# Optimization experiments

Measured on AMD Instinct MI355X. Metric: run time of the kernel, lower is better.

## Reference

```python
import jax, jax.numpy as jnp
import numpy as np

S_NUM, E_NUM, K, B = 50000, 20000, 128, 8192
N = S_NUM + E_NUM
N_EDGES = 1000000
LAYERS = 3


def setup_inputs() -> dict:
    key = jax.random.key(0)
    ks = jax.random.split(key, 16)
    return {
        "stu_emb": jax.random.normal(ks[0], (S_NUM, K), jnp.float32),
        "exer_emb": jax.random.normal(ks[1], (E_NUM, K), jnp.float32),
        "kn_emb": jax.random.normal(ks[2], (K, K), jnp.float32),
        "disc_emb": jax.random.normal(ks[3], (E_NUM, 1), jnp.float32),
        "right_W": jax.random.normal(ks[4], (LAYERS, K, K), jnp.float32) * (1.0 / np.sqrt(K)),
        "wrong_W": jax.random.normal(ks[5], (LAYERS, K, K), jnp.float32) * (1.0 / np.sqrt(K)),
        "right_ci": jax.random.uniform(ks[6], (N, 1), jnp.float32),
        "right_cj": jax.random.uniform(ks[7], (N, 1), jnp.float32),
        "wrong_ci": jax.random.uniform(ks[8], (N, 1), jnp.float32),
        "wrong_cj": jax.random.uniform(ks[9], (N, 1), jnp.float32),
        "right_edges": jax.random.randint(ks[10], (2, N_EDGES), 0, N, jnp.int64),
        "wrong_edges": jax.random.randint(ks[11], (2, N_EDGES), 0, N, jnp.int64),
        "student_id": jax.random.randint(ks[12], (B,), 0, S_NUM, jnp.int64),
        "exercise_id": jax.random.randint(ks[13], (B,), 0, E_NUM, jnp.int64),
    }


def _gcmc_layer(feat, W, cj, ci, src, dst, n_nodes):
    # dense projection + src-side normalizer (dropout is identity in eval)
    h = (feat @ W) * cj                    # [N, K]
    # copy_u/sum message passing: scatter-add messages to destination nodes
    agg = jax.ops.segment_sum(h[src], dst, num_segments=n_nodes)  # [N, K]
    return agg * ci


def _graph_forward(feat, Ws, ci, cj, edges, n_nodes):
    src, dst = edges[0], edges[1]
    for i in range(Ws.shape[0]):
        feat = _gcmc_layer(feat, Ws[i], cj, ci, src, dst, n_nodes)
    return feat


def reference(stu_emb, exer_emb, kn_emb, disc_emb, right_W, wrong_W,
              right_ci, right_cj, wrong_ci, wrong_cj,
              right_edges, wrong_edges, student_id, exercise_id):
    n_students = stu_emb.shape[0]
    n_nodes = stu_emb.shape[0] + exer_emb.shape[0]
    all_weight = jnp.concatenate([stu_emb, exer_emb], axis=0)  # [N, K]
    w1 = _graph_forward(all_weight, right_W, right_ci, right_cj, right_edges, n_nodes)
    w2 = _graph_forward(all_weight, wrong_W, wrong_ci, wrong_cj, wrong_edges, n_nodes)
    stu_forward = w1[:n_students] + w2[:n_students]
    exer_forward = w1[n_students:] + w2[n_students:]
    batch_stu_ts = stu_forward[student_id]      # [B, K]
    batch_exer_ts = exer_forward[exercise_id]   # [B, K]
    disc_ts = disc_emb[exercise_id]             # [B, 1]
    knowledge_ts = kn_emb                       # [K, K]
    return (batch_stu_ts, batch_exer_ts, disc_ts, knowledge_ts)
```

## Files before the change

kernel.cpp:

```cpp
#include <hip/hip_runtime.h>
#include <hip/hip_bf16.h>
#include <stdint.h>

#define S_NUM 50000
#define E_NUM 20000
#define NNODE 70000
#define KDIM 128
#define BATCH 8192
#define NEDGE 1000000

#define NRANGE 128
#define RSZ 547
#define BUCKET_CAP 8448
#define RCAP 16672
#define CHUNK 8192
#define BINCAP 120
#define GR 256

typedef __attribute__((ext_vector_type(8))) short short8;
typedef __attribute__((ext_vector_type(4))) float f32x4;
typedef __attribute__((ext_vector_type(2))) float f32x2;

__device__ __forceinline__ float bf2f(ushort u) {
    union { uint32_t i; float f; } v; v.i = ((uint32_t)u) << 16; return v.f;
}
__device__ __forceinline__ ushort f2bf(float f) {
    union { uint32_t i; float f; } v; v.f = f;
    uint32_t r = v.i + 0x7fffu + ((v.i >> 16) & 1u);
    return (ushort)(r >> 16);
}
__device__ __forceinline__ f32x2 up2(uint32_t u) {
    union { uint32_t i; float f; } lo, hi;
    lo.i = u << 16; hi.i = u & 0xffff0000u;
    f32x2 r; r.x = lo.f; r.y = hi.f; return r;
}

__global__ void prepW_k(const float* __restrict__ rW, const float* __restrict__ wW,
                        ushort* __restrict__ ws, int* __restrict__ gbcnt) {
    if (blockIdx.x == 0 && threadIdx.x < 256) gbcnt[threadIdx.x] = 0;
    int i = blockIdx.x * blockDim.x + threadIdx.x;
    if (i >= 6 * 16384) return;
    int m = i >> 14, idx = i & 16383;
    const float* W = (m < 3) ? rW + m * 16384 : wW + (m - 3) * 16384;
    float x = W[idx];
    int k = idx >> 7, c = idx & 127;
    ushort hb = f2bf(x);
    ushort lb = f2bf(x - bf2f(hb));
    int off = ((c * 256 + 2 * k) ^ ((c & 7) << 4)) >> 1;
    ws[(size_t)m * 32768 + off] = hb;
    ws[(size_t)m * 32768 + 16384 + off] = lb;
}

__global__ __launch_bounds__(256) void bucket_k(const int* __restrict__ redge,
                                                const int* __restrict__ wedge,
                                                int* __restrict__ gbcnt,
                                                uint32_t* __restrict__ bpk) {
    __shared__ uint32_t lpk[NRANGE][BINCAP];
    __shared__ int lcnt[NRANGE];
    __shared__ int gbase[NRANGE];
    const int NB = (NEDGE + CHUNK - 1) / CHUNK;
    int bid = blockIdx.x;
    int graph = bid >= NB;
    int cb = graph ? bid - NB : bid;
    const int* eg = graph ? wedge : redge;
    int e0 = cb * CHUNK;
    int nthis = min(CHUNK, NEDGE - e0);
    for (int i = threadIdx.x; i < NRANGE; i += 256) lcnt[i] = 0;
    __syncthreads();
    for (int i = threadIdx.x; i < nthis; i += 256) {
        int s = eg[e0 + i];
        int d = eg[NEDGE + e0 + i];
        int b = d / RSZ;
        uint32_t p = ((uint32_t)(d - b * RSZ) << 17) | (uint32_t)s;
        int slot = atomicAdd(&lcnt[b], 1);
        if (slot < BINCAP) lpk[b][slot] = p;
        else {
            int gs = atomicAdd(&gbcnt[graph * NRANGE + b], 1);
            if (gs < BUCKET_CAP)
                bpk[(size_t)(graph * NRANGE + b) * BUCKET_CAP + gs] = p;
        }
    }
    __syncthreads();
    for (int b = threadIdx.x; b < NRANGE; b += 256) {
        int c = min(lcnt[b], BINCAP);
        lcnt[b] = c;
        gbase[b] = atomicAdd(&gbcnt[graph * NRANGE + b], c);
    }
    __syncthreads();
    for (int b = 0; b < NRANGE; ++b) {
        int c = lcnt[b];
        size_t base = (size_t)(graph * NRANGE + b) * BUCKET_CAP + gbase[b];
        for (int i = threadIdx.x; i < c; i += 256)
            if (gbase[b] + i < BUCKET_CAP) bpk[base + i] = lpk[b][i];
    }
}

__global__ __launch_bounds__(256) void build_k(const uint32_t* __restrict__ bpk,
                                               const int* __restrict__ gbcnt,
                                               int* __restrict__ rpb,
                                               int* __restrict__ rpe,
                                               int* __restrict__ csr) {
    __shared__ int lcnt[RSZ];
    __shared__ int lexcl[RSZ];
    __shared__ int pexcl[RSZ];
    __shared__ int lcur[RSZ];
    __shared__ int sliceB[BUCKET_CAP];
    __shared__ int wsum[4];
    __shared__ int s_carry;
    int combo = blockIdx.x;
    int graph = combo >> 7, grp = combo & (NRANGE - 1);
    int lo = grp * RSZ;
    int rsize = min(RSZ, NNODE - lo);
    int n = min(gbcnt[combo], BUCKET_CAP);
    const uint32_t* bp = bpk + (size_t)combo * BUCKET_CAP;
    int* rpbg = rpb + graph * NNODE;
    int* rpeg = rpe + graph * NNODE;
    int* og = csr + (size_t)combo * RCAP;
    const int rbase = combo * RCAP;
    int tid = threadIdx.x, lane = tid & 63, wid = tid >> 6;

    for (int i = tid; i < rsize; i += 256) lcnt[i] = 0;
    if (tid == 0) s_carry = 0;
    __syncthreads();
    for (int i = tid; i < n; i += 256)
        atomicAdd(&lcnt[bp[i] >> 17], 1);
    __syncthreads();
    for (int base = 0; base < rsize; base += 256) {
        int i = base + tid;
        int v = (i < rsize) ? lcnt[i] : 0;
        int incl = v;
        #pragma unroll
        for (int off = 1; off < 64; off <<= 1) {
            int t = __shfl_up(incl, off, 64);
            if (lane >= off) incl += t;
        }
        if (lane == 63) wsum[wid] = incl;
        __syncthreads();
        int carry = s_carry;
        if (wid == 0 && lane < 4) {
            int wv = wsum[lane];
            #pragma unroll
            for (int off = 1; off < 4; off <<= 1) {
                int t = __shfl_up(wv, off, 64);
                if (lane >= off) wv += t;
            }
            wsum[lane] = wv;
        }
        __syncthreads();
        int waveoff = (wid == 0) ? 0 : wsum[wid - 1];
        int excl = carry + waveoff + incl - v;
        if (i < rsize) { lexcl[i] = excl; lcur[i] = excl; }
        __syncthreads();
        if (tid == 0) s_carry = carry + wsum[3];
        __syncthreads();
    }
    if (tid == 0) s_carry = 0;
    __syncthreads();
    for (int base = 0; base < rsize; base += 256) {
        int i = base + tid;
        int v = (i < rsize) ? ((lcnt[i] + 15) & ~15) : 0;
        int incl = v;
        #pragma unroll
        for (int off = 1; off < 64; off <<= 1) {
            int t = __shfl_up(incl, off, 64);
            if (lane >= off) incl += t;
        }
        if (lane == 63) wsum[wid] = incl;
        __syncthreads();
        int carry = s_carry;
        if (wid == 0 && lane < 4) {
            int wv = wsum[lane];
            #pragma unroll
            for (int off = 1; off < 4; off <<= 1) {
                int t = __shfl_up(wv, off, 64);
                if (lane >= off) wv += t;
            }
            wsum[lane] = wv;
        }
        __syncthreads();
        int waveoff = (wid == 0) ? 0 : wsum[wid - 1];
        int excl = carry + waveoff + incl - v;
        if (i < rsize) pexcl[i] = excl;
        __syncthreads();
        if (tid == 0) s_carry = carry + wsum[3];
        __syncthreads();
    }
    for (int i = tid; i < rsize; i += 256) {
        int pc = (lcnt[i] + 15) & ~15;
        rpbg[lo + i] = rbase + pexcl[i];
        rpeg[lo + i] = rbase + pexcl[i] + pc;
    }
    for (int i = tid; i < n; i += 256) {
        uint32_t p = bp[i];
        int slot = atomicAdd(&lcur[p >> 17], 1);
        sliceB[slot] = (int)p;
    }
    __syncthreads();
    for (int i = tid; i < n; i += 256) {
        uint32_t p = (uint32_t)sliceB[i];
        int r = p >> 17;
        og[pexcl[r] + (i - lexcl[r])] = (int)(p & 0x1FFFFu);
    }
    for (int r = tid; r < rsize; r += 256) {
        int c = lcnt[r], pc = (c + 15) & ~15, b = pexcl[r];
        for (int j = c; j < pc; ++j) og[b + j] = NNODE;
    }
}

__global__ __launch_bounds__(256) void cvt1_k(const float* __restrict__ stu,
                                              const float* __restrict__ exer,
                                              const float* __restrict__ rcj,
                                              const float* __restrict__ wcj,
                                              uint4* __restrict__ featb,
                                              uint4* __restrict__ fcR,
                                              uint4* __restrict__ fcW,
                                              float* __restrict__ cjpR,
                                              float* __restrict__ cjpW) {
    const int main = NNODE * 16;
    const int total = main + 48 + 2 * (NNODE + 1);
    const uint4 z4 = {0, 0, 0, 0};
    for (int i = blockIdx.x * blockDim.x + threadIdx.x; i < total;
         i += gridDim.x * blockDim.x) {
        if (i < main) {
            int node = i >> 4;
            int qq = i & 15;
            const float4* src = (const float4*)((node < S_NUM)
                                  ? stu + (size_t)node * KDIM
                                  : exer + (size_t)(node - S_NUM) * KDIM);
            float4 a = src[qq * 2];
            float4 b = src[qq * 2 + 1];
            uint4 o;
            o.x = (uint32_t)f2bf(a.x) | ((uint32_t)f2bf(a.y) << 16);
            o.y = (uint32_t)f2bf(a.z) | ((uint32_t)f2bf(a.w) << 16);
            o.z = (uint32_t)f2bf(b.x) | ((uint32_t)f2bf(b.y) << 16);
            o.w = (uint32_t)f2bf(b.z) | ((uint32_t)f2bf(b.w) << 16);
            featb[i] = o;
        } else if (i < main + 48) {
            int j = i - main;
            if (j < 16)      featb[(size_t)NNODE * 16 + j] = z4;
            else if (j < 32) fcR[(size_t)NNODE * 16 + (j - 16)] = z4;
            else             fcW[(size_t)NNODE * 16 + (j - 32)] = z4;
        } else {
            int k = i - main - 48;
            if (k <= NNODE)  cjpR[k] = (k < NNODE) ? rcj[k] : 0.f;
            else {
                int m = k - (NNODE + 1);
                cjpW[m] = (m < NNODE) ? wcj[m] : 0.f;
            }
        }
    }
}

__global__ __launch_bounds__(256) void agg2_k(const uint4* __restrict__ fcR,
                                              const uint4* __restrict__ fcW,
                                              const float* __restrict__ cjR,
                                              const float* __restrict__ cjW,
                                              const int* __restrict__ rpb,
                                              const int* __restrict__ rpe,
                                              const int* __restrict__ csr,
                                              uint4* __restrict__ outR,
                                              uint4* __restrict__ outW,
                                              int useCj) {
    int gn = (blockIdx.x * blockDim.x + threadIdx.x) >> 6;
    if (gn >= 2 * NNODE) return;
    int graph = gn >= NNODE;
    int n = graph ? gn - NNODE : gn;
    const uint4* fc = graph ? fcW : fcR;
    const float* cjg = graph ? cjW : cjR;
    const int* rpbg = rpb + graph * NNODE;
    const int* rpeg = rpe + graph * NNODE;
    uint4* outp = graph ? outW : outR;

    int lane = threadIdx.x & 63;
    int rowgrp = lane >> 4, c16 = lane & 15;
    int beg = rpbg[n], end = rpeg[n];
    f32x2 acc0 = {0.f, 0.f}, acc1 = {0.f, 0.f}, acc2v = {0.f, 0.f}, acc3 = {0.f, 0.f};

    if (useCj) {
        for (int e = beg; e < end; e += 16) {
            int s0 = csr[e + rowgrp];
            int s1 = csr[e + 4 + rowgrp];
            int s2 = csr[e + 8 + rowgrp];
            int s3 = csr[e + 12 + rowgrp];
            uint4 u0 = fc[(size_t)s0 * 16 + c16];
            uint4 u1 = fc[(size_t)s1 * 16 + c16];
            uint4 u2 = fc[(size_t)s2 * 16 + c16];
            uint4 u3 = fc[(size_t)s3 * 16 + c16];
            float c0 = cjg[s0], c1 = cjg[s1], c2 = cjg[s2], c3 = cjg[s3];
            f32x2 v0 = {c0, c0}, v1 = {c1, c1}, v2 = {c2, c2}, v3 = {c3, c3};
            acc0 += v0 * up2(u0.x) + v1 * up2(u1.x) + v2 * up2(u2.x) + v3 * up2(u3.x);
            acc1 += v0 * up2(u0.y) + v1 * up2(u1.y) + v2 * up2(u2.y) + v3 * up2(u3.y);
            acc2v += v0 * up2(u0.z) + v1 * up2(u1.z) + v2 * up2(u2.z) + v3 * up2(u3.z);
            acc3 += v0 * up2(u0.w) + v1 * up2(u1.w) + v2 * up2(u2.w) + v3 * up2(u3.w);
        }
    } else {
        for (int e = beg; e < end; e += 16) {
            int s0 = csr[e + rowgrp];
            int s1 = csr[e + 4 + rowgrp];
            int s2 = csr[e + 8 + rowgrp];
            int s3 = csr[e + 12 + rowgrp];
            uint4 u0 = fc[(size_t)s0 * 16 + c16];
            uint4 u1 = fc[(size_t)s1 * 16 + c16];
            uint4 u2 = fc[(size_t)s2 * 16 + c16];
            uint4 u3 = fc[(size_t)s3 * 16 + c16];
            acc0 += (up2(u0.x) + up2(u1.x)) + (up2(u2.x) + up2(u3.x));
            acc1 += (up2(u0.y) + up2(u1.y)) + (up2(u2.y) + up2(u3.y));
            acc2v += (up2(u0.z) + up2(u1.z)) + (up2(u2.z) + up2(u3.z));
            acc3 += (up2(u0.w) + up2(u1.w)) + (up2(u2.w) + up2(u3.w));
        }
    }
    float a[8] = {acc0.x, acc0.y, acc1.x, acc1.y, acc2v.x, acc2v.y, acc3.x, acc3.y};
    #pragma unroll
    for (int j = 0; j < 8; ++j) {
        a[j] += __shfl_xor(a[j], 16, 64);
        a[j] += __shfl_xor(a[j], 32, 64);
    }
    if (rowgrp == 0) {
        uint4 o;
        o.x = (uint32_t)f2bf(a[0]) | ((uint32_t)f2bf(a[1]) << 16);
        o.y = (uint32_t)f2bf(a[2]) | ((uint32_t)f2bf(a[3]) << 16);
        o.z = (uint32_t)f2bf(a[4]) | ((uint32_t)f2bf(a[5]) << 16);
        o.w = (uint32_t)f2bf(a[6]) | ((uint32_t)f2bf(a[7]) << 16);
        outp[(size_t)n * 16 + c16] = o;
    }
}

__global__ __launch_bounds__(256) void gemm2_k(const ushort* __restrict__ AR,
                                               const ushort* __restrict__ AW,
                                               const ushort* __restrict__ wsR,
                                               const ushort* __restrict__ wsW,
                                               const float* __restrict__ rci,
                                               const float* __restrict__ rcj,
                                               const float* __restrict__ wci,
                                               const float* __restrict__ wcj,
                                               ushort* __restrict__ outR,
                                               ushort* __restrict__ outW,
                                               int mode) {
    const int halfBlocks = (NNODE + GR - 1) / GR;
    int graph = blockIdx.x >= halfBlocks;
    int bb = graph ? blockIdx.x - halfBlocks : blockIdx.x;
    const ushort* A = graph ? AW : AR;
    const ushort* wsm = graph ? wsW : wsR;
    const float* ci = graph ? wci : rci;
    const float* cj = graph ? wcj : rcj;
    ushort* outB = graph ? outW : outR;

    __shared__ ushort wt[32768];
    {
        const uint4* g = (const uint4*)wsm;
        uint4* l = (uint4*)wt;
        for (int i = threadIdx.x; i < 4096; i += 256) l[i] = g[i];
    }
    __syncthreads();

    int wid = threadIdx.x >> 6, lane = threadIdx.x & 63;
    int q = lane >> 4, l16 = lane & 15;
    int rbase = bb * GR + wid * 64;

    short8 z8 = {0, 0, 0, 0, 0, 0, 0, 0};
    short8 afr[4][4];
    #pragma unroll
    for (int t = 0; t < 4; ++t) {
        int row = rbase + t * 16 + l16;
        bool rok = row < NNODE;
        const short8* ar = (const short8*)(A + (size_t)row * KDIM);
        #pragma unroll
        for (int kb = 0; kb < 4; ++kb)
            afr[t][kb] = rok ? ar[kb * 4 + q] : z8;
    }
    float scal[4][4];
    #pragma unroll
    for (int t = 0; t < 4; ++t)
        #pragma unroll
        for (int b = 0; b < 4; ++b) {
            int r = rbase + t * 16 + q * 4 + b;
            scal[t][b] = (r < NNODE) ? (mode ? ci[r] * cj[r] : ci[r]) : 0.f;
        }

    #pragma unroll
    for (int cb = 0; cb < 8; ++cb) {
        int c = cb * 16 + l16;
        short8 bHi[4], bLo[4];
        #pragma unroll
        for (int kb = 0; kb < 4; ++kb) {
            int byte = (c * 256 + 2 * (kb * 32 + q * 8)) ^ ((c & 7) << 4);
            bHi[kb] = *(const short8*)((const char*)wt + byte);
            bLo[kb] = *(const short8*)((const char*)wt + 32768 + byte);
        }
        #pragma unroll
        for (int t = 0; t < 4; ++t) {
            f32x4 acc = {0.f, 0.f, 0.f, 0.f};
            #pragma unroll
            for (int kb = 0; kb < 4; ++kb) {
                acc = __builtin_amdgcn_mfma_f32_16x16x32_bf16(afr[t][kb], bHi[kb], acc, 0, 0, 0);
                acc = __builtin_amdgcn_mfma_f32_16x16x32_bf16(afr[t][kb], bLo[kb], acc, 0, 0, 0);
            }
            #pragma unroll
            for (int b = 0; b < 4; ++b) {
                int r = rbase + t * 16 + q * 4 + b;
                if (r < NNODE)
                    outB[(size_t)r * KDIM + c] = f2bf(acc[b] * scal[t][b]);
            }
        }
    }
}

__global__ void out_k(const ushort* __restrict__ w1, const ushort* __restrict__ w2,
                      const float* __restrict__ disc, const float* __restrict__ kn,
                      const int* __restrict__ sid, const int* __restrict__ eid,
                      float* __restrict__ out) {
    const int total = 2 * BATCH * KDIM + BATCH + KDIM * KDIM;
    for (int i = blockIdx.x * blockDim.x + threadIdx.x; i < total;
         i += gridDim.x * blockDim.x) {
        if (i < BATCH * KDIM) {
            int b = i >> 7, c = i & 127;
            size_t n = (size_t)sid[b];
            out[i] = bf2f(w1[n * KDIM + c]) + bf2f(w2[n * KDIM + c]);
        } else if (i < 2 * BATCH * KDIM) {
            int j = i - BATCH * KDIM;
            int b = j >> 7, c = j & 127;
            size_t n = (size_t)(S_NUM + eid[b]);
            out[i] = bf2f(w1[n * KDIM + c]) + bf2f(w2[n * KDIM + c]);
        } else if (i < 2 * BATCH * KDIM + BATCH) {
            out[i] = disc[eid[i - 2 * BATCH * KDIM]];
        } else {
            out[i] = kn[i - (2 * BATCH * KDIM + BATCH)];
        }
    }
}

static inline size_t align_up(size_t x) { return (x + 255) & ~(size_t)255; }

extern "C" void kernel_launch(void* const* d_in, const int* in_sizes, int n_in,
                              void* d_out, int out_size, void* d_ws, size_t ws_size,
                              hipStream_t stream) {
    const float* stu  = (const float*)d_in[0];
    const float* exer = (const float*)d_in[1];
    const float* kn   = (const float*)d_in[2];
    const float* disc = (const float*)d_in[3];
    const float* rW   = (const float*)d_in[4];
    const float* wW   = (const float*)d_in[5];
    const float* rci  = (const float*)d_in[6];
    const float* rcj  = (const float*)d_in[7];
    const float* wci  = (const float*)d_in[8];
    const float* wcj  = (const float*)d_in[9];
    const int* redge   = (const int*)d_in[10];
    const int* wedge   = (const int*)d_in[11];
    const int* sid     = (const int*)d_in[12];
    const int* eid     = (const int*)d_in[13];
    float* out         = (float*)d_out;

    char* p = (char*)d_ws;
    const size_t fB16 = align_up((size_t)(NNODE + 1) * KDIM * 2);
    ushort* featb = (ushort*)p; p += fB16;
    ushort* fcR = (ushort*)p; p += fB16;
    ushort* fcW = (ushort*)p; p += fB16;
    ushort* pR  = (ushort*)p; p += fB16;
    ushort* pW  = (ushort*)p; p += fB16;
    ushort* ws  = (ushort*)p; p += align_up((size_t)6 * 32768 * 2);
    int* gbcnt = (int*)p; p += align_up((size_t)256 * 4);
    int* rpb = (int*)p; p += align_up((size_t)2 * NNODE * 4);
    int* rpe = (int*)p; p += align_up((size_t)2 * NNODE * 4);
    int* csr = (int*)p; p += align_up((size_t)256 * RCAP * 4);
    float* cjpR = (float*)p; p += align_up((size_t)(NNODE + 1) * 4);
    float* cjpW = (float*)p; p += align_up((size_t)(NNODE + 1) * 4);
    uint32_t* bpk = (uint32_t*)pR;

    const int gemmBlocks2 = 2 * ((NNODE + GR - 1) / GR);
    const int aggBlocks2 = (2 * NNODE * 64) / 256;
    const int NB = (NEDGE + CHUNK - 1) / CHUNK;

    prepW_k<<<(6 * 16384 + 255) / 256, 256, 0, stream>>>(rW, wW, ws, gbcnt);
    bucket_k<<<2 * NB, 256, 0, stream>>>(redge, wedge, gbcnt, bpk);
    build_k<<<256, 256, 0, stream>>>(bpk, gbcnt, rpb, rpe, csr);
    cvt1_k<<<2048, 256, 0, stream>>>(stu, exer, rcj, wcj, (uint4*)featb,
                                     (uint4*)fcR, (uint4*)fcW, cjpR, cjpW);

    agg2_k<<<aggBlocks2, 256, 0, stream>>>((const uint4*)featb, (const uint4*)featb,
                                           cjpR, cjpW, rpb, rpe, csr,
                                           (uint4*)pR, (uint4*)pW, 1);
    gemm2_k<<<gemmBlocks2, 256, 0, stream>>>(pR, pW, ws + 0 * 32768, ws + 3 * 32768,
                                             rci, rcj, wci, wcj, fcR, fcW, 1);
    agg2_k<<<aggBlocks2, 256, 0, stream>>>((const uint4*)fcR, (const uint4*)fcW,
                                           nullptr, nullptr, rpb, rpe, csr,
                                           (uint4*)pR, (uint4*)pW, 0);
    gemm2_k<<<gemmBlocks2, 256, 0, stream>>>(pR, pW, ws + 1 * 32768, ws + 4 * 32768,
                                             rci, rcj, wci, wcj, fcR, fcW, 1);
    agg2_k<<<aggBlocks2, 256, 0, stream>>>((const uint4*)fcR, (const uint4*)fcW,
                                           nullptr, nullptr, rpb, rpe, csr,
                                           (uint4*)pR, (uint4*)pW, 0);
    gemm2_k<<<gemmBlocks2, 256, 0, stream>>>(pR, pW, ws + 2 * 32768, ws + 5 * 32768,
                                             rci, rcj, wci, wcj, fcR, fcW, 0);

    out_k<<<2048, 256, 0, stream>>>(fcR, fcW, disc, kn, sid, eid, out);
}
```

Measured before the change: 393.7 us.

## Fuse neighbor aggregation with per-node MFMA projection into one kernel per layer

Each layer previously ran a gather/aggregate kernel writing bf16 rows to global memory, then a separate GEMM kernel reading them back. The new aggemm_k has each wave aggregate 16 nodes (two at a time, interleaving their edge gathers for more memory parallelism), stage the results in a swizzled LDS tile, and immediately multiply by the layer weight with MFMA. Weights are now read from global memory instead of being copied into LDS per block. This removes one intermediate write and read plus three launches, but each wave does a small 16-row GEMM with weight reloads, and uneven node degrees within a wave may cause imbalance. Ping-pong buffers swap between pR/pW and fcR/fcW, so their padding rows are now zeroed as well.

Result: slower. 406.0 us (+3.1%).

```diff
diff --git a/kernel.cpp b/kernel.cpp
--- a/kernel.cpp
+++ b/kernel.cpp
@@ -15,7 +15,6 @@
 #define RCAP 16672
 #define CHUNK 8192
 #define BINCAP 120
-#define GR 256
 
 typedef __attribute__((ext_vector_type(8))) short short8;
 typedef __attribute__((ext_vector_type(4))) float f32x4;
@@ -214,10 +213,12 @@
                                               uint4* __restrict__ featb,
                                               uint4* __restrict__ fcR,
                                               uint4* __restrict__ fcW,
+                                              uint4* __restrict__ pR,
+                                              uint4* __restrict__ pW,
                                               float* __restrict__ cjpR,
                                               float* __restrict__ cjpW) {
     const int main = NNODE * 16;
-    const int total = main + 48 + 2 * (NNODE + 1);
+    const int total = main + 80 + 2 * (NNODE + 1);
     const uint4 z4 = {0, 0, 0, 0};
     for (int i = blockIdx.x * blockDim.x + threadIdx.x; i < total;
          i += gridDim.x * blockDim.x) {
@@ -235,13 +236,18 @@
             o.z = (uint32_t)f2bf(b.x) | ((uint32_t)f2bf(b.y) << 16);
             o.w = (uint32_t)f2bf(b.z) | ((uint32_t)f2bf(b.w) << 16);
             featb[i] = o;
-        } else if (i < main + 48) {
+        } else if (i < main + 80) {
             int j = i - main;
-            if (j < 16)      featb[(size_t)NNODE * 16 + j] = z4;
-            else if (j < 32) fcR[(size_t)NNODE * 16 + (j - 16)] = z4;
-            else             fcW[(size_t)NNODE * 16 + (j - 32)] = z4;
+            size_t off = (size_t)NNODE * 16 + (j & 15);
+            switch (j >> 4) {
+                case 0: featb[off] = z4; break;
+                case 1: fcR[off] = z4; break;
+                case 2: fcW[off] = z4; break;
+                case 3: pR[off] = z4; break;
+                default: pW[off] = z4; break;
+            }
         } else {
-            int k = i - main - 48;
+            int k = i - main - 80;
             if (k <= NNODE)  cjpR[k] = (k < NNODE) ? rcj[k] : 0.f;
             else {
                 int m = k - (NNODE + 1);
@@ -251,156 +257,139 @@
     }
 }
 
-__global__ __launch_bounds__(256) void agg2_k(const uint4* __restrict__ fcR,
-                                              const uint4* __restrict__ fcW,
-                                              const float* __restrict__ cjR,
-                                              const float* __restrict__ cjW,
-                                              const int* __restrict__ rpb,
-                                              const int* __restrict__ rpe,
-                                              const int* __restrict__ csr,
-                                              uint4* __restrict__ outR,
-                                              uint4* __restrict__ outW,
-                                              int useCj) {
-    int gn = (blockIdx.x * blockDim.x + threadIdx.x) >> 6;
-    if (gn >= 2 * NNODE) return;
-    int graph = gn >= NNODE;
-    int n = graph ? gn - NNODE : gn;
-    const uint4* fc = graph ? fcW : fcR;
+template<int USECJ>
+__device__ __forceinline__ void gath4(const uint4* __restrict__ fc,
+                                      const float* __restrict__ cjg,
+                                      const int* __restrict__ csr,
+                                      int e, int rowgrp, int c16,
+                                      f32x2& a0, f32x2& a1, f32x2& a2, f32x2& a3) {
+    int s0 = csr[e + rowgrp];
+    int s1 = csr[e + 4 + rowgrp];
+    int s2 = csr[e + 8 + rowgrp];
+    int s3 = csr[e + 12 + rowgrp];
+    uint4 u0 = fc[(size_t)s0 * 16 + c16];
+    uint4 u1 = fc[(size_t)s1 * 16 + c16];
+    uint4 u2 = fc[(size_t)s2 * 16 + c16];
+    uint4 u3 = fc[(size_t)s3 * 16 + c16];
+    if (USECJ) {
+        float c0 = cjg[s0], c1 = cjg[s1], c2 = cjg[s2], c3 = cjg[s3];
+        f32x2 v0 = {c0, c0}, v1 = {c1, c1}, v2 = {c2, c2}, v3 = {c3, c3};
+        a0 += v0 * up2(u0.x) + v1 * up2(u1.x) + v2 * up2(u2.x) + v3 * up2(u3.x);
+        a1 += v0 * up2(u0.y) + v1 * up2(u1.y) + v2 * up2(u2.y) + v3 * up2(u3.y);
+        a2 += v0 * up2(u0.z) + v1 * up2(u1.z) + v2 * up2(u2.z) + v3 * up2(u3.z);
+        a3 += v0 * up2(u0.w) + v1 * up2(u1.w) + v2 * up2(u2.w) + v3 * up2(u3.w);
+    } else {
+        a0 += (up2(u0.x) + up2(u1.x)) + (up2(u2.x) + up2(u3.x));
+        a1 += (up2(u0.y) + up2(u1.y)) + (up2(u2.y) + up2(u3.y));
+        a2 += (up2(u0.z) + up2(u1.z)) + (up2(u2.z) + up2(u3.z));
+        a3 += (up2(u0.w) + up2(u1.w)) + (up2(u2.w) + up2(u3.w));
+    }
+}
+
+template<int USECJ>
+__global__ __launch_bounds__(256) void aggemm_k(const uint4* __restrict__ srcR,
+                                                const uint4* __restrict__ srcW,
+                                                const float* __restrict__ cjR,
+                                                const float* __restrict__ cjW,
+                                                const int* __restrict__ rpb,
+                                                const int* __restrict__ rpe,
+                                                const int* __restrict__ csr,
+                                                const ushort* __restrict__ wsR,
+                                                const ushort* __restrict__ wsW,
+                                                const float* __restrict__ rci,
+                                                const float* __restrict__ rcj,
+                                                const float* __restrict__ wci,
+                                                const float* __restrict__ wcj,
+                                                ushort* __restrict__ outR,
+                                                ushort* __restrict__ outW,
+                                                int mode) {
+    __shared__ char stage[4][4096];
+    const int BPG = (NNODE + 63) / 64;
+    int graph = blockIdx.x >= BPG;
+    int bb = graph ? blockIdx.x - BPG : blockIdx.x;
+    const uint4* fc = graph ? srcW : srcR;
     const float* cjg = graph ? cjW : cjR;
     const int* rpbg = rpb + graph * NNODE;
     const int* rpeg = rpe + graph * NNODE;
-    uint4* outp = graph ? outW : outR;
-
-    int lane = threadIdx.x & 63;
+    const ushort* wsm = graph ? wsW : wsR;
+    const float* cia = graph ? wci : rci;
+    const float* cja = graph ? wcj : rcj;
+    ushort* outB = graph ? outW : outR;
+
+    int wid = threadIdx.x >> 6, lane = threadIdx.x & 63;
     int rowgrp = lane >> 4, c16 = lane & 15;
-    int beg = rpbg[n], end = rpeg[n];
-    f32x2 acc0 = {0.f, 0.f}, acc1 = {0.f, 0.f}, acc2v = {0.f, 0.f}, acc3 = {0.f, 0.f};
-
-    if (useCj) {
-        for (int e = beg; e < end; e += 16) {
-            int s0 = csr[e + rowgrp];
-            int s1 = csr[e + 4 + rowgrp];
-            int s2 = csr[e + 8 + rowgrp];
-            int s3 = csr[e + 12 + rowgrp];
-            uint4 u0 = fc[(size_t)s0 * 16 + c16];
-            uint4 u1 = fc[(size_t)s1 * 16 + c16];
-            uint4 u2 = fc[(size_t)s2 * 16 + c16];
-            uint4 u3 = fc[(size_t)s3 * 16 + c16];
-            float c0 = cjg[s0], c1 = cjg[s1], c2 = cjg[s2], c3 = cjg[s3];
-            f32x2 v0 = {c0, c0}, v1 = {c1, c1}, v2 = {c2, c2}, v3 = {c3, c3};
-            acc0 += v0 * up2(u0.x) + v1 * up2(u1.x) + v2 * up2(u2.x) + v3 * up2(u3.x);
-            acc1 += v0 * up2(u0.y) + v1 * up2(u1.y) + v2 * up2(u2.y) + v3 * up2(u3.y);
-            acc2v += v0 * up2(u0.z) + v1 * up2(u1.z) + v2 * up2(u2.z) + v3 * up2(u3.z);
-            acc3 += v0 * up2(u0.w) + v1 * up2(u1.w) + v2 * up2(u2.w) + v3 * up2(u3.w);
-        }
-    } else {
-        for (int e = beg; e < end; e += 16) {
-            int s0 = csr[e + rowgrp];
-            int s1 = csr[e + 4 + rowgrp];
-            int s2 = csr[e + 8 + rowgrp];
-            int s3 = csr[e + 12 + rowgrp];
-            uint4 u0 = fc[(size_t)s0 * 16 + c16];
-            uint4 u1 = fc[(size_t)s1 * 16 + c16];
-            uint4 u2 = fc[(size_t)s2 * 16 + c16];
-            uint4 u3 = fc[(size_t)s3 * 16 + c16];
-            acc0 += (up2(u0.x) + up2(u1.x)) + (up2(u2.x) + up2(u3.x));
-            acc1 += (up2(u0.y) + up2(u1.y)) + (up2(u2.y) + up2(u3.y));
-            acc2v += (up2(u0.z) + up2(u1.z)) + (up2(u2.z) + up2(u3.z));
-            acc3 += (up2(u0.w) + up2(u1.w)) + (up2(u2.w) + up2(u3.w));
-        }
-    }
-    float a[8] = {acc0.x, acc0.y, acc1.x, acc1.y, acc2v.x, acc2v.y, acc3.x, acc3.y};
+    int nodebase = bb * 64 + wid * 16;
+    char* st = stage[wid];
+
+    for (int nl = 0; nl < 16; nl += 2) {
+        int nA = nodebase + nl, nB = nA + 1;
+        f32x2 aA0 = {0.f, 0.f}, aA1 = {0.f, 0.f}, aA2 = {0.f, 0.f}, aA3 = {0.f, 0.f};
+        f32x2 aB0 = {0.f, 0.f}, aB1 = {0.f, 0.f}, aB2 = {0.f, 0.f}, aB3 = {0.f, 0.f};
+        int eA = 0, endA = 0, eB = 0, endB = 0;
+        if (nA < NNODE) { eA = rpbg[nA]; endA = rpeg[nA]; }
+        if (nB < NNODE) { eB = rpbg[nB]; endB = rpeg[nB]; }
+        while (eA < endA || eB < endB) {
+            if (eA < endA) {
+                gath4<USECJ>(fc, cjg, csr, eA, rowgrp, c16, aA0, aA1, aA2, aA3);
+                eA += 16;
+            }
+            if (eB < endB) {
+                gath4<USECJ>(fc, cjg, csr, eB, rowgrp, c16, aB0, aB1, aB2, aB3);
+                eB += 16;
+            }
+        }
+        float rA[8] = {aA0.x, aA0.y, aA1.x, aA1.y, aA2.x, aA2.y, aA3.x, aA3.y};
+        float rB[8] = {aB0.x, aB0.y, aB1.x, aB1.y, aB2.x, aB2.y, aB3.x, aB3.y};
+        #pragma unroll
+        for (int j = 0; j < 8; ++j) {
+            rA[j] += __shfl_xor(rA[j], 16, 64);
+            rA[j] += __shfl_xor(rA[j], 32, 64);
+            rB[j] += __shfl_xor(rB[j], 16, 64);
+            rB[j] += __shfl_xor(rB[j], 32, 64);
+        }
+        if (rowgrp == 0) {
+            uint4 oA, oB;
+            oA.x = (uint32_t)f2bf(rA[0]) | ((uint32_t)f2bf(rA[1]) << 16);
+            oA.y = (uint32_t)f2bf(rA[2]) | ((uint32_t)f2bf(rA[3]) << 16);
+            oA.z = (uint32_t)f2bf(rA[4]) | ((uint32_t)f2bf(rA[5]) << 16);
+            oA.w = (uint32_t)f2bf(rA[6]) | ((uint32_t)f2bf(rA[7]) << 16);
+            oB.x = (uint32_t)f2bf(rB[0]) | ((uint32_t)f2bf(rB[1]) << 16);
+            oB.y = (uint32_t)f2bf(rB[2]) | ((uint32_t)f2bf(rB[3]) << 16);
+            oB.z = (uint32_t)f2bf(rB[4]) | ((uint32_t)f2bf(rB[5]) << 16);
+            oB.w = (uint32_t)f2bf(rB[6]) | ((uint32_t)f2bf(rB[7]) << 16);
+            *(uint4*)(st + nl * 256 + ((c16 ^ (nl & 7)) << 4)) = oA;
+            *(uint4*)(st + (nl + 1) * 256 + ((c16 ^ ((nl + 1) & 7)) << 4)) = oB;
+        }
+    }
+
+    int q = rowgrp, l16 = c16;
+    short8 afr[4];
     #pragma unroll
-    for (int j = 0; j < 8; ++j) {
-        a[j] += __shfl_xor(a[j], 16, 64);
-        a[j] += __shfl_xor(a[j], 32, 64);
-    }
-    if (rowgrp == 0) {
-        uint4 o;
-        o.x = (uint32_t)f2bf(a[0]) | ((uint32_t)f2bf(a[1]) << 16);
-        o.y = (uint32_t)f2bf(a[2]) | ((uint32_t)f2bf(a[3]) << 16);
-        o.z = (uint32_t)f2bf(a[4]) | ((uint32_t)f2bf(a[5]) << 16);
-        o.w = (uint32_t)f2bf(a[6]) | ((uint32_t)f2bf(a[7]) << 16);
-        outp[(size_t)n * 16 + c16] = o;
-    }
-}
-
-__global__ __launch_bounds__(256) void gemm2_k(const ushort* __restrict__ AR,
-                                               const ushort* __restrict__ AW,
-                                               const ushort* __restrict__ wsR,
-                                               const ushort* __restrict__ wsW,
-                                               const float* __restrict__ rci,
-                                               const float* __restrict__ rcj,
-                                               const float* __restrict__ wci,
-                                               const float* __restrict__ wcj,
-                                               ushort* __restrict__ outR,
-                                               ushort* __restrict__ outW,
-                                               int mode) {
-    const int halfBlocks = (NNODE + GR - 1) / GR;
-    int graph = blockIdx.x >= halfBlocks;
-    int bb = graph ? blockIdx.x - halfBlocks : blockIdx.x;
-    const ushort* A = graph ? AW : AR;
-    const ushort* wsm = graph ? wsW : wsR;
-    const float* ci = graph ? wci : rci;
-    const float* cj = graph ? wcj : rcj;
-    ushort* outB = graph ? outW : outR;
-
-    __shared__ ushort wt[32768];
-    {
-        const uint4* g = (const uint4*)wsm;
-        uint4* l = (uint4*)wt;
-        for (int i = threadIdx.x; i < 4096; i += 256) l[i] = g[i];
-    }
-    __syncthreads();
-
-    int wid = threadIdx.x >> 6, lane = threadIdx.x & 63;
-    int q = lane >> 4, l16 = lane & 15;
-    int rbase = bb * GR + wid * 64;
-
-    short8 z8 = {0, 0, 0, 0, 0, 0, 0, 0};
-    short8 afr[4][4];
+    for (int kb = 0; kb < 4; ++kb)
+        afr[kb] = *(const short8*)(st + l16 * 256 + ((((kb << 2) + q) ^ (l16 & 7)) << 4));
+    float scal[4];
     #pragma unroll
-    for (int t = 0; t < 4; ++t) {
-        int row = rbase + t * 16 + l16;
-        bool rok = row < NNODE;
-        const short8* ar = (const short8*)(A + (size_t)row * KDIM);
-        #pragma unroll
-        for (int kb = 0; kb < 4; ++kb)
-            afr[t][kb] = rok ? ar[kb * 4 + q] : z8;
-    }
-    float scal[4][4];
-    #pragma unroll
-    for (int t = 0; t < 4; ++t)
-        #pragma unroll
-        for (int b = 0; b < 4; ++b) {
-            int r = rbase + t * 16 + q * 4 + b;
-            scal[t][b] = (r < NNODE) ? (mode ? ci[r] * cj[r] : ci[r]) : 0.f;
-        }
-
+    for (int b = 0; b < 4; ++b) {
+        int r = nodebase + q * 4 + b;
+        scal[b] = (r < NNODE) ? (mode ? cia[r] * cja[r] : cia[r]) : 0.f;
+    }
     #pragma unroll
     for (int cb = 0; cb < 8; ++cb) {
         int c = cb * 16 + l16;
-        short8 bHi[4], bLo[4];
+        f32x4 acc = {0.f, 0.f, 0.f, 0.f};
         #pragma unroll
         for (int kb = 0; kb < 4; ++kb) {
             int byte = (c * 256 + 2 * (kb * 32 + q * 8)) ^ ((c & 7) << 4);
-            bHi[kb] = *(const short8*)((const char*)wt + byte);
-            bLo[kb] = *(const short8*)((const char*)wt + 32768 + byte);
+            short8 bHi = *(const short8*)((const char*)wsm + byte);
+            short8 bLo = *(const short8*)((const char*)wsm + 32768 + byte);
+            acc = __builtin_amdgcn_mfma_f32_16x16x32_bf16(afr[kb], bHi, acc, 0, 0, 0);
+            acc = __builtin_amdgcn_mfma_f32_16x16x32_bf16(afr[kb], bLo, acc, 0, 0, 0);
         }
         #pragma unroll
-        for (int t = 0; t < 4; ++t) {
-            f32x4 acc = {0.f, 0.f, 0.f, 0.f};
-            #pragma unroll
-            for (int kb = 0; kb < 4; ++kb) {
-                acc = __builtin_amdgcn_mfma_f32_16x16x32_bf16(afr[t][kb], bHi[kb], acc, 0, 0, 0);
-                acc = __builtin_amdgcn_mfma_f32_16x16x32_bf16(afr[t][kb], bLo[kb], acc, 0, 0, 0);
-            }
-            #pragma unroll
-            for (int b = 0; b < 4; ++b) {
-                int r = rbase + t * 16 + q * 4 + b;
-                if (r < NNODE)
-                    outB[(size_t)r * KDIM + c] = f2bf(acc[b] * scal[t][b]);
-            }
+        for (int b = 0; b < 4; ++b) {
+            int r = nodebase + q * 4 + b;
+            if (r < NNODE)
+                outB[(size_t)r * KDIM + c] = f2bf(acc[b] * scal[b]);
         }
     }
 }
@@ -466,31 +455,28 @@
     float* cjpW = (float*)p; p += align_up((size_t)(NNODE + 1) * 4);
     uint32_t* bpk = (uint32_t*)pR;
 
-    const int gemmBlocks2 = 2 * ((NNODE + GR - 1) / GR);
-    const int aggBlocks2 = (2 * NNODE * 64) / 256;
+    const int agBlocks = 2 * ((NNODE + 63) / 64);
     const int NB = (NEDGE + CHUNK - 1) / CHUNK;
 
     prepW_k<<<(6 * 16384 + 255) / 256, 256, 0, stream>>>(rW, wW, ws, gbcnt);
     bucket_k<<<2 * NB, 256, 0, stream>>>(redge, wedge, gbcnt, bpk);
     build_k<<<256, 256, 0, stream>>>(bpk, gbcnt, rpb, rpe, csr);
     cvt1_k<<<2048, 256, 0, stream>>>(stu, exer, rcj, wcj, (uint4*)featb,
-                                     (uint4*)fcR, (uint4*)fcW, cjpR, cjpW);
-
-    agg2_k<<<aggBlocks2, 256, 0, stream>>>((const uint4*)featb, (const uint4*)featb,
-                                           cjpR, cjpW, rpb, rpe, csr,
-                                           (uint4*)pR, (uint4*)pW, 1);
-    gemm2_k<<<gemmBlocks2, 256, 0, stream>>>(pR, pW, ws + 0 * 32768, ws + 3 * 32768,
-                                             rci, rcj, wci, wcj, fcR, fcW, 1);
-    agg2_k<<<aggBlocks2, 256, 0, stream>>>((const uint4*)fcR, (const uint4*)fcW,
-                                           nullptr, nullptr, rpb, rpe, csr,
-                                           (uint4*)pR, (uint4*)pW, 0);
-    gemm2_k<<<gemmBlocks2, 256, 0, stream>>>(pR, pW, ws + 1 * 32768, ws + 4 * 32768,
-                                             rci, rcj, wci, wcj, fcR, fcW, 1);
-    agg2_k<<<aggBlocks2, 256, 0, stream>>>((const uint4*)fcR, (const uint4*)fcW,
-                                           nullptr, nullptr, rpb, rpe, csr,
-                                           (uint4*)pR, (uint4*)pW, 0);
-    gemm2_k<<<gemmBlocks2, 256, 0, stream>>>(pR, pW, ws + 2 * 32768, ws + 5 * 32768,
-                                             rci, rcj, wci, wcj, fcR, fcW, 0);
-
-    out_k<<<2048, 256, 0, stream>>>(fcR, fcW, disc, kn, sid, eid, out);
-}
+                                     (uint4*)fcR, (uint4*)fcW, (uint4*)pR, (uint4*)pW,
+                                     cjpR, cjpW);
+
+    aggemm_k<1><<<agBlocks, 256, 0, stream>>>((const uint4*)featb, (const uint4*)featb,
+                                              cjpR, cjpW, rpb, rpe, csr,
+                                              ws + 0 * 32768, ws + 3 * 32768,
+                                              rci, rcj, wci, wcj, pR, pW, 1);
+    aggemm_k<0><<<agBlocks, 256, 0, stream>>>((const uint4*)pR, (const uint4*)pW,
+                                              nullptr, nullptr, rpb, rpe, csr,
+                                              ws + 1 * 32768, ws + 4 * 32768,
+                                              rci, rcj, wci, wcj, fcR, fcW, 1);
+    aggemm_k<0><<<agBlocks, 256, 0, stream>>>((const uint4*)fcR, (const uint4*)fcW,
+                                              nullptr, nullptr, rpb, rpe, csr,
+                                              ws + 2 * 32768, ws + 5 * 32768,
+                                              rci, rcj, wci, wcj, pR, pW, 0);
+
+    out_k<<<2048, 256, 0, stream>>>(pR, pW, disc, kn, sid, eid, out);
+}
```

## Compute final GCN layer only for batch-referenced nodes via compaction

Applied to the files above, without the earlier changes.

Marks the nodes referenced by the student and exercise ids, compacts them into a list with a single-block prefix scan, and runs the last aggregation and GEMM only on those rows, writing them to compact buffers that out_k reads through an inverse map. The aggregation kernel is also restructured so that each 16-lane group owns one node and processes 8 edges per iteration, which removes the cross-group shuffle reduction. This is meant to skip most of the final-layer work, since the batch touches at most about 16K of the 70K nodes. It adds mark and compact kernels, and the compact kernel runs serially on a single block.

Measured after the change: 405.2 us. 2.9% more time.

```diff
diff --git a/kernel.cpp b/kernel.cpp
--- a/kernel.cpp
+++ b/kernel.cpp
@@ -16,6 +16,7 @@
 #define CHUNK 8192
 #define BINCAP 120
 #define GR 256
+#define CAPC 16384
 
 typedef __attribute__((ext_vector_type(8))) short short8;
 typedef __attribute__((ext_vector_type(4))) float f32x4;
@@ -36,11 +37,13 @@
 }
 
 __global__ void prepW_k(const float* __restrict__ rW, const float* __restrict__ wW,
-                        ushort* __restrict__ ws, int* __restrict__ gbcnt) {
+                        ushort* __restrict__ ws, int* __restrict__ gbcnt,
+                        int* __restrict__ flags) {
+    int t = blockIdx.x * blockDim.x + threadIdx.x;
     if (blockIdx.x == 0 && threadIdx.x < 256) gbcnt[threadIdx.x] = 0;
-    int i = blockIdx.x * blockDim.x + threadIdx.x;
-    if (i >= 6 * 16384) return;
-    int m = i >> 14, idx = i & 16383;
+    if (t < NNODE) flags[t] = 0;
+    if (t >= 6 * 16384) return;
+    int m = t >> 14, idx = t & 16383;
     const float* W = (m < 3) ? rW + m * 16384 : wW + (m - 3) * 16384;
     float x = W[idx];
     int k = idx >> 7, c = idx & 127;
@@ -205,6 +208,54 @@
         int c = lcnt[r], pc = (c + 15) & ~15, b = pexcl[r];
         for (int j = c; j < pc; ++j) og[b + j] = NNODE;
     }
+}
+
+__global__ void mark_k(const int* __restrict__ sid, const int* __restrict__ eid,
+                       int* __restrict__ flags) {
+    int i = blockIdx.x * blockDim.x + threadIdx.x;
+    if (i < BATCH) flags[sid[i]] = 1;
+    else if (i < 2 * BATCH) flags[S_NUM + eid[i - BATCH]] = 1;
+}
+
+__global__ __launch_bounds__(1024) void compact_k(const int* __restrict__ flags,
+                                                  int* __restrict__ list,
+                                                  int* __restrict__ inv,
+                                                  int* __restrict__ nsel) {
+    __shared__ int wsum[16];
+    __shared__ int s_carry;
+    int tid = threadIdx.x, lane = tid & 63, wid = tid >> 6;
+    if (tid == 0) s_carry = 0;
+    __syncthreads();
+    for (int base = 0; base < NNODE; base += 1024) {
+        int i = base + tid;
+        int v = (i < NNODE) ? flags[i] : 0;
+        int incl = v;
+        #pragma unroll
+        for (int off = 1; off < 64; off <<= 1) {
+            int t = __shfl_up(incl, off, 64);
+            if (lane >= off) incl += t;
+        }
+        if (lane == 63) wsum[wid] = incl;
+        __syncthreads();
+        int carry = s_carry;
+        if (wid == 0 && lane < 16) {
+            int wv = wsum[lane];
+            #pragma unroll
+            for (int off = 1; off < 16; off <<= 1) {
+                int t = __shfl_up(wv, off, 64);
+                if (lane >= off) wv += t;
+            }
+            wsum[lane] = wv;
+        }
+        __syncthreads();
+        int waveoff = (wid == 0) ? 0 : wsum[wid - 1];
+        int excl = carry + waveoff + incl - v;
+        if (i < NNODE && v) { list[excl] = i; inv[i] = excl; }
+        __syncthreads();
+        if (tid == 0) s_carry = carry + wsum[15];
+        __syncthreads();
+    }
+    if (tid == 0) nsel[0] = s_carry;
 }
 
 __global__ __launch_bounds__(256) void cvt1_k(const float* __restrict__ stu,
@@ -237,9 +288,12 @@
             featb[i] = o;
         } else if (i < main + 48) {
             int j = i - main;
-            if (j < 16)      featb[(size_t)NNODE * 16 + j] = z4;
-            else if (j < 32) fcR[(size_t)NNODE * 16 + (j - 16)] = z4;
-            else             fcW[(size_t)NNODE * 16 + (j - 32)] = z4;
+            size_t off = (size_t)NNODE * 16 + (j & 15);
+            switch (j >> 4) {
+                case 0: featb[off] = z4; break;
+                case 1: fcR[off] = z4; break;
+                default: fcW[off] = z4; break;
+            }
         } else {
             int k = i - main - 48;
             if (k <= NNODE)  cjpR[k] = (k < NNODE) ? rcj[k] : 0.f;
@@ -251,80 +305,86 @@
     }
 }
 
-__global__ __launch_bounds__(256) void agg2_k(const uint4* __restrict__ fcR,
-                                              const uint4* __restrict__ fcW,
+template<int USECJ, int COMPACT>
+__global__ __launch_bounds__(256) void agg2_k(const uint4* __restrict__ srcR,
+                                              const uint4* __restrict__ srcW,
                                               const float* __restrict__ cjR,
                                               const float* __restrict__ cjW,
                                               const int* __restrict__ rpb,
                                               const int* __restrict__ rpe,
                                               const int* __restrict__ csr,
+                                              const int* __restrict__ list,
+                                              const int* __restrict__ nselp,
                                               uint4* __restrict__ outR,
-                                              uint4* __restrict__ outW,
-                                              int useCj) {
-    int gn = (blockIdx.x * blockDim.x + threadIdx.x) >> 6;
-    if (gn >= 2 * NNODE) return;
-    int graph = gn >= NNODE;
-    int n = graph ? gn - NNODE : gn;
-    const uint4* fc = graph ? fcW : fcR;
+                                              uint4* __restrict__ outW) {
+    int lane = threadIdx.x & 63, wid = threadIdx.x >> 6;
+    int grp = lane >> 4, c16 = lane & 15;
+    int gi = blockIdx.x * 16 + wid * 4 + grp;
+    int graph, n, orow;
+    if (COMPACT) {
+        int nsel = nselp[0];
+        graph = gi >= CAPC;
+        int ci = graph ? gi - CAPC : gi;
+        if (ci >= nsel) return;
+        n = list[ci];
+        orow = ci;
+    } else {
+        if (gi >= 2 * NNODE) return;
+        graph = gi >= NNODE;
+        n = graph ? gi - NNODE : gi;
+        orow = n;
+    }
+    const uint4* fc = graph ? srcW : srcR;
     const float* cjg = graph ? cjW : cjR;
-    const int* rpbg = rpb + graph * NNODE;
-    const int* rpeg = rpe + graph * NNODE;
+    int beg = (rpb + graph * NNODE)[n];
+    int end = (rpe + graph * NNODE)[n];
     uint4* outp = graph ? outW : outR;
 
-    int lane = threadIdx.x & 63;
-    int rowgrp = lane >> 4, c16 = lane & 15;
-    int beg = rpbg[n], end = rpeg[n];
-    f32x2 acc0 = {0.f, 0.f}, acc1 = {0.f, 0.f}, acc2v = {0.f, 0.f}, acc3 = {0.f, 0.f};
-
-    if (useCj) {
-        for (int e = beg; e < end; e += 16) {
-            int s0 = csr[e + rowgrp];
-            int s1 = csr[e + 4 + rowgrp];
-            int s2 = csr[e + 8 + rowgrp];
-            int s3 = csr[e + 12 + rowgrp];
-            uint4 u0 = fc[(size_t)s0 * 16 + c16];
-            uint4 u1 = fc[(size_t)s1 * 16 + c16];
-            uint4 u2 = fc[(size_t)s2 * 16 + c16];
-            uint4 u3 = fc[(size_t)s3 * 16 + c16];
+    f32x2 a0 = {0.f, 0.f}, a1 = {0.f, 0.f}, a2 = {0.f, 0.f}, a3 = {0.f, 0.f};
+    for (int e = beg; e < end; e += 8) {
+        int s0 = csr[e],     s1 = csr[e + 1], s2 = csr[e + 2], s3 = csr[e + 3];
+        int s4 = csr[e + 4], s5 = csr[e + 5], s6 = csr[e + 6], s7 = csr[e + 7];
+        uint4 u0 = fc[(size_t)s0 * 16 + c16];
+        uint4 u1 = fc[(size_t)s1 * 16 + c16];
+        uint4 u2 = fc[(size_t)s2 * 16 + c16];
+        uint4 u3 = fc[(size_t)s3 * 16 + c16];
+        uint4 u4 = fc[(size_t)s4 * 16 + c16];
+        uint4 u5 = fc[(size_t)s5 * 16 + c16];
+        uint4 u6 = fc[(size_t)s6 * 16 + c16];
+        uint4 u7 = fc[(size_t)s7 * 16 + c16];
+        if (USECJ) {
             float c0 = cjg[s0], c1 = cjg[s1], c2 = cjg[s2], c3 = cjg[s3];
+            float c4 = cjg[s4], c5 = cjg[s5], c6 = cjg[s6], c7 = cjg[s7];
             f32x2 v0 = {c0, c0}, v1 = {c1, c1}, v2 = {c2, c2}, v3 = {c3, c3};
-            acc0 += v0 * up2(u0.x) + v1 * up2(u1.x) + v2 * up2(u2.x) + v3 * up2(u3.x);
-            acc1 += v0 * up2(u0.y) + v1 * up2(u1.y) + v2 * up2(u2.y) + v3 * up2(u3.y);
-            acc2v += v0 * up2(u0.z) + v1 * up2(u1.z) + v2 * up2(u2.z) + v3 * up2(u3.z);
-            acc3 += v0 * up2(u0.w) + v1 * up2(u1.w) + v2 * up2(u2.w) + v3 * up2(u3.w);
-        }
-    } else {
-        for (int e = beg; e < end; e += 16) {
-            int s0 = csr[e + rowgrp];
-            int s1 = csr[e + 4 + rowgrp];
-            int s2 = csr[e + 8 + rowgrp];
-            int s3 = csr[e + 12 + rowgrp];
-            uint4 u0 = fc[(size_t)s0 * 16 + c16];
-            uint4 u1 = fc[(size_t)s1 * 16 + c16];
-            uint4 u2 = fc[(size_t)s2 * 16 + c16];
-            uint4 u3 = fc[(size_t)s3 * 16 + c16];
-            acc0 += (up2(u0.x) + up2(u1.x)) + (up2(u2.x) + up2(u3.x));
-            acc1 += (up2(u0.y) + up2(u1.y)) + (up2(u2.y) + up2(u3.y));
-            acc2v += (up2(u0.z) + up2(u1.z)) + (up2(u2.z) + up2(u3.z));
-            acc3 += (up2(u0.w) + up2(u1.w)) + (up2(u2.w) + up2(u3.w));
-        }
-    }
-    float a[8] = {acc0.x, acc0.y, acc1.x, acc1.y, acc2v.x, acc2v.y, acc3.x, acc3.y};
-    #pragma unroll
-    for (int j = 0; j < 8; ++j) {
-        a[j] += __shfl_xor(a[j], 16, 64);
-        a[j] += __shfl_xor(a[j], 32, 64);
-    }
-    if (rowgrp == 0) {
-        uint4 o;
-        o.x = (uint32_t)f2bf(a[0]) | ((uint32_t)f2bf(a[1]) << 16);
-        o.y = (uint32_t)f2bf(a[2]) | ((uint32_t)f2bf(a[3]) << 16);
-        o.z = (uint32_t)f2bf(a[4]) | ((uint32_t)f2bf(a[5]) << 16);
-        o.w = (uint32_t)f2bf(a[6]) | ((uint32_t)f2bf(a[7]) << 16);
-        outp[(size_t)n * 16 + c16] = o;
-    }
-}
-
+            f32x2 v4 = {c4, c4}, v5 = {c5, c5}, v6 = {c6, c6}, v7 = {c7, c7};
+            a0 += v0 * up2(u0.x) + v1 * up2(u1.x) + v2 * up2(u2.x) + v3 * up2(u3.x)
+                + v4 * up2(u4.x) + v5 * up2(u5.x) + v6 * up2(u6.x) + v7 * up2(u7.x);
+            a1 += v0 * up2(u0.y) + v1 * up2(u1.y) + v2 * up2(u2.y) + v3 * up2(u3.y)
+                + v4 * up2(u4.y) + v5 * up2(u5.y) + v6 * up2(u6.y) + v7 * up2(u7.y);
+            a2 += v0 * up2(u0.z) + v1 * up2(u1.z) + v2 * up2(u2.z) + v3 * up2(u3.z)
+                + v4 * up2(u4.z) + v5 * up2(u5.z) + v6 * up2(u6.z) + v7 * up2(u7.z);
+            a3 += v0 * up2(u0.w) + v1 * up2(u1.w) + v2 * up2(u2.w) + v3 * up2(u3.w)
+                + v4 * up2(u4.w) + v5 * up2(u5.w) + v6 * up2(u6.w) + v7 * up2(u7.w);
+        } else {
+            a0 += (up2(u0.x) + up2(u1.x)) + (up2(u2.x) + up2(u3.x))
+                + (up2(u4.x) + up2(u5.x)) + (up2(u6.x) + up2(u7.x));
+            a1 += (up2(u0.y) + up2(u1.y)) + (up2(u2.y) + up2(u3.y))
+                + (up2(u4.y) + up2(u5.y)) + (up2(u6.y) + up2(u7.y));
+            a2 += (up2(u0.z) + up2(u1.z)) + (up2(u2.z) + up2(u3.z))
+                + (up2(u4.z) + up2(u5.z)) + (up2(u6.z) + up2(u7.z));
+            a3 += (up2(u0.w) + up2(u1.w)) + (up2(u2.w) + up2(u3.w))
+                + (up2(u4.w) + up2(u5.w)) + (up2(u6.w) + up2(u7.w));
+        }
+    }
+    uint4 o;
+    o.x = (uint32_t)f2bf(a0.x) | ((uint32_t)f2bf(a0.y) << 16);
+    o.y = (uint32_t)f2bf(a1.x) | ((uint32_t)f2bf(a1.y) << 16);
+    o.z = (uint32_t)f2bf(a2.x) | ((uint32_t)f2bf(a2.y) << 16);
+    o.w = (uint32_t)f2bf(a3.x) | ((uint32_t)f2bf(a3.y) << 16);
+    outp[(size_t)orow * 16 + c16] = o;
+}
+
+template<int COMPACT>
 __global__ __launch_bounds__(256) void gemm2_k(const ushort* __restrict__ AR,
                                                const ushort* __restrict__ AW,
                                                const ushort* __restrict__ wsR,
@@ -333,12 +393,15 @@
                                                const float* __restrict__ rcj,
                                                const float* __restrict__ wci,
                                                const float* __restrict__ wcj,
+                                               const int* __restrict__ list,
+                                               const int* __restrict__ nselp,
                                                ushort* __restrict__ outR,
                                                ushort* __restrict__ outW,
                                                int mode) {
-    const int halfBlocks = (NNODE + GR - 1) / GR;
+    const int halfBlocks = COMPACT ? (CAPC / GR) : ((NNODE + GR - 1) / GR);
     int graph = blockIdx.x >= halfBlocks;
     int bb = graph ? blockIdx.x - halfBlocks : blockIdx.x;
+    int nrows = COMPACT ? nselp[0] : NNODE;
     const ushort* A = graph ? AW : AR;
     const ushort* wsm = graph ? wsW : wsR;
     const float* ci = graph ? wci : rci;
@@ -356,13 +419,14 @@
     int wid = threadIdx.x >> 6, lane = threadIdx.x & 63;
     int q = lane >> 4, l16 = lane & 15;
     int rbase = bb * GR + wid * 64;
+    if (rbase >= nrows) return;
 
     short8 z8 = {0, 0, 0, 0, 0, 0, 0, 0};
     short8 afr[4][4];
     #pragma unroll
     for (int t = 0; t < 4; ++t) {
         int row = rbase + t * 16 + l16;
-        bool rok = row < NNODE;
+        bool rok = row < nrows;
         const short8* ar = (const short8*)(A + (size_t)row * KDIM);
         #pragma unroll
         for (int kb = 0; kb < 4; ++kb)
@@ -374,7 +438,9 @@
         #pragma unroll
         for (int b = 0; b < 4; ++b) {
             int r = rbase + t * 16 + q * 4 + b;
-            scal[t][b] = (r < NNODE) ? (mode ? ci[r] * cj[r] : ci[r]) : 0.f;
+            bool ok = r < nrows;
+            int node = COMPACT ? (ok ? list[r] : 0) : r;
+            scal[t][b] = ok ? (mode ? ci[node] * cj[node] : ci[node]) : 0.f;
         }
 
     #pragma unroll
@@ -398,14 +464,15 @@
             #pragma unroll
             for (int b = 0; b < 4; ++b) {
                 int r = rbase + t * 16 + q * 4 + b;
-                if (r < NNODE)
+                if (r < nrows)
                     outB[(size_t)r * KDIM + c] = f2bf(acc[b] * scal[t][b]);
             }
         }
     }
 }
 
-__global__ void out_k(const ushort* __restrict__ w1, const ushort* __restrict__ w2,
+__global__ void out_k(const ushort* __restrict__ w1c, const ushort* __restrict__ w2c,
+                      const int* __restrict__ inv,
                       const float* __restrict__ disc, const float* __restrict__ kn,
                       const int* __restrict__ sid, const int* __restrict__ eid,
                       float* __restrict__ out) {
@@ -414,13 +481,13 @@
          i += gridDim.x * blockDim.x) {
         if (i < BATCH * KDIM) {
             int b = i >> 7, c = i & 127;
-            size_t n = (size_t)sid[b];
-            out[i] = bf2f(w1[n * KDIM + c]) + bf2f(w2[n * KDIM + c]);
+            size_t r = (size_t)inv[sid[b]];
+            out[i] = bf2f(w1c[r * KDIM + c]) + bf2f(w2c[r * KDIM + c]);
         } else if (i < 2 * BATCH * KDIM) {
             int j = i - BATCH * KDIM;
             int b = j >> 7, c = j & 127;
-            size_t n = (size_t)(S_NUM + eid[b]);
-            out[i] = bf2f(w1[n * KDIM + c]) + bf2f(w2[n * KDIM + c]);
+            size_t r = (size_t)inv[S_NUM + eid[b]];
+            out[i] = bf2f(w1c[r * KDIM + c]) + bf2f(w2c[r * KDIM + c]);
         } else if (i < 2 * BATCH * KDIM + BATCH) {
             out[i] = disc[eid[i - 2 * BATCH * KDIM]];
         } else {
@@ -464,33 +531,46 @@
     int* csr = (int*)p; p += align_up((size_t)256 * RCAP * 4);
     float* cjpR = (float*)p; p += align_up((size_t)(NNODE + 1) * 4);
     float* cjpW = (float*)p; p += align_up((size_t)(NNODE + 1) * 4);
+    int* flags = (int*)p; p += align_up((size_t)NNODE * 4);
+    int* list  = (int*)p; p += align_up((size_t)CAPC * 4);
+    int* inv   = (int*)p; p += align_up((size_t)NNODE * 4);
+    int* nsel  = (int*)p; p += align_up((size_t)16 * 4);
     uint32_t* bpk = (uint32_t*)pR;
-
-    const int gemmBlocks2 = 2 * ((NNODE + GR - 1) / GR);
-    const int aggBlocks2 = (2 * NNODE * 64) / 256;
+    ushort* w1c = featb;
+    ushort* w2c = featb + (size_t)CAPC * KDIM;
+
+    const int aggFull = (2 * NNODE + 15) / 16;
+    const int aggComp = 2 * CAPC / 16;
+    const int gemmFull = 2 * ((NNODE + GR - 1) / GR);
+    const int gemmComp = 2 * (CAPC / GR);
     const int NB = (NEDGE + CHUNK - 1) / CHUNK;
 
-    prepW_k<<<(6 * 16384 + 255) / 256, 256, 0, stream>>>(rW, wW, ws, gbcnt);
+    prepW_k<<<(6 * 16384 + 255) / 256, 256, 0, stream>>>(rW, wW, ws, gbcnt, flags);
     bucket_k<<<2 * NB, 256, 0, stream>>>(redge, wedge, gbcnt, bpk);
     build_k<<<256, 256, 0, stream>>>(bpk, gbcnt, rpb, rpe, csr);
+    mark_k<<<(2 * BATCH + 255) / 256, 256, 0, stream>>>(sid, eid, flags);
+    compact_k<<<1, 1024, 0, stream>>>(flags, list, inv, nsel);
     cvt1_k<<<2048, 256, 0, stream>>>(stu, exer, rcj, wcj, (uint4*)featb,
                                      (uint4*)fcR, (uint4*)fcW, cjpR, cjpW);
 
-    agg2_k<<<aggBlocks2, 256, 0, stream>>>((const uint4*)featb, (const uint4*)featb,
-                                           cjpR, cjpW, rpb, rpe, csr,
-                                           (uint4*)pR, (uint4*)pW, 1);
-    gemm2_k<<<gemmBlocks2, 256, 0, stream>>>(pR, pW, ws + 0 * 32768, ws + 3 * 32768,
-                                             rci, rcj, wci, wcj, fcR, fcW, 1);
-    agg2_k<<<aggBlocks2, 256, 0, stream>>>((const uint4*)fcR, (const uint4*)fcW,
-                                           nullptr, nullptr, rpb, rpe, csr,
-                                           (uint4*)pR, (uint4*)pW, 0);
-    gemm2_k<<<gemmBlocks2, 256, 0, stream>>>(pR, pW, ws + 1 * 32768, ws + 4 * 32768,
-                                             rci, rcj, wci, wcj, fcR, fcW, 1);
-    agg2_k<<<aggBlocks2, 256, 0, stream>>>((const uint4*)fcR, (const uint4*)fcW,
-                                           nullptr, nullptr, rpb, rpe, csr,
-                                           (uint4*)pR, (uint4*)pW, 0);
-    gemm2_k<<<gemmBlocks2, 256, 0, stream>>>(pR, pW, ws + 2 * 32768, ws + 5 * 32768,
-                                             rci, rcj, wci, wcj, fcR, fcW, 0);
-
-    out_k<<<2048, 256, 0, stream>>>(fcR, fcW, disc, kn, sid, eid, out);
-}
+    agg2_k<1, 0><<<aggFull, 256, 0, stream>>>((const uint4*)featb, (const uint4*)featb,
+                                              cjpR, cjpW, rpb, rpe, csr, nullptr, nullptr,
+                                              (uint4*)pR, (uint4*)pW);
+    gemm2_k<0><<<gemmFull, 256, 0, stream>>>(pR, pW, ws + 0 * 32768, ws + 3 * 32768,
+                                             rci, rcj, wci, wcj, nullptr, nullptr,
+                                             fcR, fcW, 1);
+    agg2_k<0, 0><<<aggFull, 256, 0, stream>>>((const uint4*)fcR, (const uint4*)fcW,
+                                              nullptr, nullptr, rpb, rpe, csr,
+                                              nullptr, nullptr, (uint4*)pR, (uint4*)pW);
+    gemm2_k<0><<<gemmFull, 256, 0, stream>>>(pR, pW, ws + 1 * 32768, ws + 4 * 32768,
+                                             rci, rcj, wci, wcj, nullptr, nullptr,
+                                             fcR, fcW, 1);
+    agg2_k<0, 1><<<aggComp, 256, 0, stream>>>((const uint4*)fcR, (const uint4*)fcW,
+                                              nullptr, nullptr, rpb, rpe, csr,
+                                              list, nsel, (uint4*)pR, (uint4*)pW);
+    gemm2_k<1><<<gemmComp, 256, 0, stream>>>(pR, pW, ws + 2 * 32768, ws + 5 * 32768,
+                                             rci, rcj, wci, wcj, list, nsel,
+                                             w1c, w2c, 0);
+
+    out_k<<<2048, 256, 0, stream>>>(w1c, w2c, inv, disc, kn, sid, eid, out);
+}
```
